# Optimization experiments

Measured on AMD Instinct MI355X. Metric: run time of the kernel, lower is better.

The kernel has to match this reference:

```python
import jax, jax.numpy as jnp
import numpy as np

B, S, HID = 2, 2048, 4096
NH, NKV = 32, 8
HD = HID // NH          # 128
GROUPS = NH // NKV      # 4


def rotate_half(x):
    x1, x2 = x[..., : x.shape[-1] // 2], x[..., x.shape[-1] // 2 :]
    return jnp.concatenate((-x2, x1), axis=-1)


def apply_rope(x, cos, sin):
    # x: (B,H,S,D); cos/sin: (B,S,D) -> (B,1,S,D)
    c = cos[:, None, :, :]
    s = sin[:, None, :, :]
    return x * c + rotate_half(x) * s


def setup_inputs() -> dict:
    key = jax.random.key(0)
    ks = jax.random.split(key, 12)
    scale = 1.0 / np.sqrt(HID)
    return {
        "hidden_states": jax.random.normal(ks[0], (B, S, HID), jnp.float32),
        "cos": jax.random.uniform(ks[1], (B, S, HD), jnp.float32),
        "sin": jax.random.uniform(ks[2], (B, S, HD), jnp.float32),
        "Wq": jax.random.normal(ks[3], (HID, NH * HD), jnp.float32) * scale,
        "bq": jax.random.normal(ks[4], (NH * HD,), jnp.float32) * 0.01,
        "Wk": jax.random.normal(ks[5], (HID, NKV * HD), jnp.float32) * scale,
        "bk": jax.random.normal(ks[6], (NKV * HD,), jnp.float32) * 0.01,
        "Wv": jax.random.normal(ks[7], (HID, NKV * HD), jnp.float32) * scale,
        "bv": jax.random.normal(ks[8], (NKV * HD,), jnp.float32) * 0.01,
        "Wo": jax.random.normal(ks[9], (NH * HD, HID), jnp.float32) * scale,
    }


def reference(hidden_states, cos, sin, Wq, bq, Wk, bk, Wv, bv, Wo):
    b, s, _ = hidden_states.shape
    q = (hidden_states @ Wq + bq).reshape(b, s, NH, HD).transpose(0, 2, 1, 3)
    k = (hidden_states @ Wk + bk).reshape(b, s, NKV, HD).transpose(0, 2, 1, 3)
    v = (hidden_states @ Wv + bv).reshape(b, s, NKV, HD).transpose(0, 2, 1, 3)
    q = apply_rope(q, cos, sin)
    k = apply_rope(k, cos, sin)
    # GQA: repeat_interleave along head dim
    k = jnp.repeat(k, GROUPS, axis=1)
    v = jnp.repeat(v, GROUPS, axis=1)
    scores = jnp.einsum("bhqd,bhkd->bhqk", q, k) / np.sqrt(HD).astype(np.float32)
    weights = jax.nn.softmax(scores, axis=-1)  # NOTE: no causal mask, per source
    out = jnp.einsum("bhqk,bhkd->bhqd", weights, v)
    out = out.transpose(0, 2, 1, 3).reshape(b, s, NH * HD)
    return out @ Wo
```

## Files before the change

kernel.cpp:

```cpp
#include <hip/hip_runtime.h>
#include <stdint.h>

#define Bz   2
#define Ss   2048
#define HID  4096
#define NH   32
#define NKV  8
#define HD   128
#define Mrows (Bz*Ss)
#define NQKV 6144

typedef __attribute__((ext_vector_type(8))) short b16x8;
typedef __attribute__((ext_vector_type(8))) _Float16 f16x8;
typedef __attribute__((ext_vector_type(4))) float f32x4;

__device__ __forceinline__ unsigned short f2bf(float f) {
  union { float f; uint32_t u; } v; v.f = f;
  uint32_t r = v.u + 0x7FFFu + ((v.u >> 16) & 1u);
  return (unsigned short)(r >> 16);
}

__device__ __forceinline__ void cp16(const void* g, void* l) {
  __builtin_amdgcn_global_load_lds(
      (const __attribute__((address_space(1))) void*)g,
      (__attribute__((address_space(3))) void*)l, 16, 0, 0);
}

__global__ __launch_bounds__(256) void cast_x(const float* __restrict__ x,
                                              unsigned short* __restrict__ o) {
  int i = blockIdx.x*256 + threadIdx.x;
  float4 v = ((const float4*)x)[i];
  ushort4 r; r.x = f2bf(v.x); r.y = f2bf(v.y); r.z = f2bf(v.z); r.w = f2bf(v.w);
  ((ushort4*)o)[i] = r;
}

__global__ __launch_bounds__(256) void wtrans(const float* __restrict__ W,
                                              unsigned short* __restrict__ Wt,
                                              int K, int N) {
  __shared__ float t[32][33];
  int n0 = blockIdx.x*32, k0 = blockIdx.y*32;
  int tx = threadIdx.x & 31, ty = threadIdx.x >> 5;
#pragma unroll
  for (int i = 0; i < 4; i++)
    t[ty + i*8][tx] = W[(size_t)(k0 + ty + i*8)*N + n0 + tx];
  __syncthreads();
#pragma unroll
  for (int i = 0; i < 4; i++)
    Wt[(size_t)(n0 + ty + i*8)*K + k0 + tx] = f2bf(t[tx][ty + i*8]);
}

__global__ __launch_bounds__(256) void bias_cat(const float* __restrict__ bq,
                                                const float* __restrict__ bk,
                                                const float* __restrict__ bv,
                                                float* __restrict__ o) {
  int i = blockIdx.x*256 + threadIdx.x;
  float v = (i < 4096) ? bq[i] : (i < 5120) ? bk[i-4096] : bv[i-5120];
  o[i] = v;
}

__global__ __launch_bounds__(256) void gemm_bt(const unsigned short* __restrict__ A,
                                               const unsigned short* __restrict__ Bt,
                                               const float* __restrict__ bias,
                                               float* __restrict__ C,
                                               int N, int K) {
  __shared__ short Al[128*32];
  __shared__ short Bl[128*32];
  const int tid = threadIdx.x;
  const int m0 = blockIdx.y * 128, n0 = blockIdx.x * 128;
  const int w = tid >> 6, lane = tid & 63;
  const int wy = w >> 1, wx = w & 1;
  const int lrow = lane & 15, quad = lane >> 4;
  const int wb = tid & 192;
  const int swz = (lrow >> 1) & 3;
  f32x4 acc[4][4] = {};
  for (int kk = 0; kk < K; kk += 32) {
    __syncthreads();
#pragma unroll
    for (int i = 0; i < 2; i++) {
      int c = i*256 + tid;
      int r = c >> 2, gc = (c & 3) ^ ((r >> 1) & 3);
      int cb = i*256 + wb;
      cp16(A  + (size_t)(m0 + r)*K + kk + gc*8, Al + cb*8);
      cp16(Bt + (size_t)(n0 + r)*K + kk + gc*8, Bl + cb*8);
    }
    __syncthreads();
    b16x8 af[4], bfr[4];
#pragma unroll
    for (int m = 0; m < 4; m++)
      af[m] = *(const b16x8*)(Al + (wy*64 + m*16 + lrow)*32 + (quad ^ swz)*8);
#pragma unroll
    for (int n = 0; n < 4; n++)
      bfr[n] = *(const b16x8*)(Bl + (wx*64 + n*16 + lrow)*32 + (quad ^ swz)*8);
#pragma unroll
    for (int m = 0; m < 4; m++)
#pragma unroll
      for (int n = 0; n < 4; n++)
        acc[m][n] = __builtin_amdgcn_mfma_f32_16x16x32_bf16(af[m], bfr[n], acc[m][n], 0, 0, 0);
  }
#pragma unroll
  for (int m = 0; m < 4; m++)
#pragma unroll
    for (int n = 0; n < 4; n++) {
      int col = n0 + wx*64 + n*16 + lrow;
      float bv = bias ? bias[col] : 0.0f;
#pragma unroll
      for (int r = 0; r < 4; r++) {
        int row = m0 + wy*64 + m*16 + quad*4 + r;
        C[(size_t)row*N + col] = acc[m][n][r] + bv;
      }
    }
}

__global__ __launch_bounds__(256) void rope(const float* __restrict__ X, int xstride, int colbase,
                                            const float* __restrict__ cp,
                                            const float* __restrict__ sp,
                                            unsigned short* __restrict__ o, int nh, float scale) {
  int tid = blockIdx.x*256 + threadIdx.x;
  int d = tid & 63;
  int h = (tid >> 6) % nh;
  int m = tid / (64*nh);
  int b = m >> 11, s = m & 2047;
  size_t xoff = (size_t)m*xstride + colbase + (size_t)h*HD + d;
  float x1 = X[xoff], x2 = X[xoff + 64];
  const float* cb = cp + ((size_t)b*Ss + s)*HD;
  const float* sb = sp + ((size_t)b*Ss + s)*HD;
  float o1 = (x1*cb[d]      - x2*sb[d])      * scale;
  float o2 = (x2*cb[d + 64] + x1*sb[d + 64]) * scale;
  unsigned short* ob = o + ((size_t)(b*nh + h)*Ss + s)*HD;
  ob[d]      = f2bf(o1);
  ob[d + 64] = f2bf(o2);
}

__global__ __launch_bounds__(256) void vprep(const float* __restrict__ Vf, int xstride, int colbase,
                                             _Float16* __restrict__ Vt) {
  __shared__ float t[32][33];
  int dt = blockIdx.x, st = blockIdx.y, bk = blockIdx.z;
  int b = bk >> 3, kvh = bk & 7;
  int tx = threadIdx.x & 31, ty = threadIdx.x >> 5;
#pragma unroll
  for (int i = 0; i < 4; i++) {
    int s = st*32 + ty + i*8;
    t[ty + i*8][tx] = Vf[(size_t)(b*Ss + s)*xstride + colbase + kvh*HD + dt*32 + tx];
  }
  __syncthreads();
#pragma unroll
  for (int i = 0; i < 4; i++) {
    int d = dt*32 + ty + i*8;
    Vt[((size_t)bk*HD + d)*Ss + st*32 + tx] = (_Float16)t[tx][ty + i*8];
  }
}

__global__ __launch_bounds__(256) void flash(const unsigned short* __restrict__ Qr,
                                             const unsigned short* __restrict__ Kr,
                                             const _Float16* __restrict__ Vt,
                                             unsigned short* __restrict__ AO) {
  __shared__ short Kl[64*128];
  __shared__ short Vl[144*64];
  __shared__ _Float16 Pl[4][16*72];
  const int qt = blockIdx.x, h = blockIdx.y, b = blockIdx.z;
  const int tid = threadIdx.x, w = tid >> 6, lane = tid & 63;
  const int lrow = lane & 15, quad = lane >> 4;
  const int wb = tid & 192;
  const int swz = lrow & 7;
  const int kvh = h >> 2;
  const unsigned short* Qb = Qr + ((size_t)(b*NH + h)*Ss + qt*64 + w*16)*HD;
  const unsigned short* Kb = Kr + ((size_t)(b*NKV + kvh)*Ss)*HD;
  const _Float16*       Vb = Vt + ((size_t)(b*NKV + kvh)*HD)*Ss;
  {
    int idx = tid*4;
    int row = 128 + (idx >> 6);
    unsigned short v = (row == 128) ? 0x3C00u : 0u;
    ushort4 vv; vv.x = v; vv.y = v; vv.z = v; vv.w = v;
    *(ushort4*)((unsigned short*)Vl + 128*64 + idx) = vv;
  }
  b16x8 qf[4];
#pragma unroll
  for (int t = 0; t < 4; t++)
    qf[t] = *(const b16x8*)(Qb + (size_t)lrow*HD + t*32 + quad*8);
  f32x4 o[8] = {};
  f32x4 ol = {};
  for (int kt = 0; kt < 32; kt++) {
    __syncthreads();
#pragma unroll
    for (int i = 0; i < 4; i++) {
      int c = i*256 + tid;
      int r = c >> 4, gc = (c & 15) ^ (r & 7);
      cp16(Kb + (size_t)(kt*64 + r)*HD + gc*8, Kl + (i*256 + wb)*8);
    }
#pragma unroll
    for (int i = 0; i < 4; i++) {
      int c = i*256 + tid;
      int r = c >> 3, gc = (c & 7) ^ (r & 7);
      cp16(Vb + (size_t)r*Ss + kt*64 + gc*8, Vl + (i*256 + wb)*8);
    }
    __syncthreads();
    f32x4 sc[4] = {};
#pragma unroll
    for (int t = 0; t < 4; t++)
#pragma unroll
      for (int n = 0; n < 4; n++) {
        b16x8 kf = *(const b16x8*)(Kl + (n*16 + lrow)*128 + ((t*4 + quad) ^ swz)*8);
        sc[n] = __builtin_amdgcn_mfma_f32_16x16x32_bf16(qf[t], kf, sc[n], 0, 0, 0);
      }
#pragma unroll
    for (int n = 0; n < 4; n++)
#pragma unroll
      for (int r = 0; r < 4; r++)
        Pl[w][(quad*4 + r)*72 + n*16 + lrow] = (_Float16)__builtin_amdgcn_exp2f(sc[n][r]);
#pragma unroll
    for (int st = 0; st < 2; st++) {
      f16x8 pf = *(const f16x8*)(&Pl[w][lrow*72 + st*32 + quad*8]);
#pragma unroll
      for (int n = 0; n < 8; n++) {
        f16x8 vf = *(const f16x8*)((const _Float16*)Vl + (n*16 + lrow)*64 + ((st*4 + quad) ^ swz)*8);
        o[n] = __builtin_amdgcn_mfma_f32_16x16x32_f16(pf, vf, o[n], 0, 0, 0);
      }
      f16x8 vf1 = *(const f16x8*)((const _Float16*)Vl + (128 + lrow)*64 + ((st*4 + quad) ^ swz)*8);
      ol = __builtin_amdgcn_mfma_f32_16x16x32_f16(pf, vf1, ol, 0, 0, 0);
    }
  }
  float rl[4];
#pragma unroll
  for (int r = 0; r < 4; r++)
    rl[r] = 1.0f / __shfl(ol[r], lane & 48);
  const int s0 = qt*64 + w*16;
#pragma unroll
  for (int n = 0; n < 8; n++)
#pragma unroll
    for (int r = 0; r < 4; r++) {
      int srow = s0 + quad*4 + r;
      float v = o[n][r] * rl[r];
      AO[((size_t)(b*Ss + srow))*HID + h*HD + n*16 + lrow] = f2bf(v);
    }
}

extern "C" void kernel_launch(void* const* d_in, const int* in_sizes, int n_in,
                              void* d_out, int out_size, void* d_ws, size_t ws_size,
                              hipStream_t stream) {
  (void)in_sizes; (void)n_in; (void)out_size; (void)ws_size;
  const float* hs   = (const float*)d_in[0];
  const float* cosp = (const float*)d_in[1];
  const float* sinp = (const float*)d_in[2];
  const float* Wq   = (const float*)d_in[3];
  const float* bq   = (const float*)d_in[4];
  const float* Wk   = (const float*)d_in[5];
  const float* bk   = (const float*)d_in[6];
  const float* Wv   = (const float*)d_in[7];
  const float* bv   = (const float*)d_in[8];
  const float* Wo   = (const float*)d_in[9];
  float* out = (float*)d_out;
  const float QSC = 0.12751742826919558f;

  char* p = (char*)d_ws;
  unsigned short* Xb   = (unsigned short*)p; p += (size_t)Mrows*HID*2;
  unsigned short* Wcat = (unsigned short*)p; p += (size_t)NQKV*HID*2;
  unsigned short* Wot  = (unsigned short*)p; p += (size_t)HID*HID*2;
  float* bcat = (float*)p; p += (size_t)NQKV*4;
  float* QKVf = (float*)p; p += (size_t)Mrows*NQKV*4;
  unsigned short* Qr = Xb;
  unsigned short* Kr = Wcat;
  _Float16*       Vt = (_Float16*)(Wcat + (size_t)(Bz*NKV)*Ss*HD);
  unsigned short* AO = (unsigned short*)QKVf;

  cast_x<<<Mrows*HID/1024, 256, 0, stream>>>(hs, Xb);
  wtrans<<<dim3(HID/32, HID/32),      256, 0, stream>>>(Wq, Wcat,                        HID, HID);
  wtrans<<<dim3((NKV*HD)/32, HID/32), 256, 0, stream>>>(Wk, Wcat + (size_t)4096*HID,     HID, NKV*HD);
  wtrans<<<dim3((NKV*HD)/32, HID/32), 256, 0, stream>>>(Wv, Wcat + (size_t)5120*HID,     HID, NKV*HD);
  wtrans<<<dim3(HID/32, HID/32),      256, 0, stream>>>(Wo, Wot, HID, HID);
  bias_cat<<<NQKV/256, 256, 0, stream>>>(bq, bk, bv, bcat);

  gemm_bt<<<dim3(NQKV/128, Mrows/128), 256, 0, stream>>>(Xb, Wcat, bcat, QKVf, NQKV, HID);

  rope<<<(Mrows*NH*64)/256,  256, 0, stream>>>(QKVf, NQKV, 0,    cosp, sinp, Qr, NH,  QSC);
  rope<<<(Mrows*NKV*64)/256, 256, 0, stream>>>(QKVf, NQKV, 4096, cosp, sinp, Kr, NKV, 1.0f);
  vprep<<<dim3(HD/32, Ss/32, Bz*NKV), 256, 0, stream>>>(QKVf, NQKV, 5120, Vt);

  flash<<<dim3(Ss/64, NH, Bz), 256, 0, stream>>>(Qr, Kr, Vt, AO);

  gemm_bt<<<dim3(HID/128, Mrows/128), 256, 0, stream>>>(AO, Wot, nullptr, out, HID, HID);
}
```

Baseline: 975.0 us.

## Rewrite GEMM with 256x256 tiles, double-buffered LDS, and XCD-aware block remap

The bf16 GEMM is restructured to use 512-thread blocks computing 256x256 output tiles with K-step 64. LDS is double-buffered so global-to-LDS async copies for tile t+2 overlap the MFMA work on the current tile, with explicit waitcnt and barriers. Block IDs are remapped across the eight XCDs to improve L2 locality, and setprio raises priority around the MFMA bursts. The larger tile increases register pressure (a 32-accumulator array per wave) and LDS use (128KB per block), which could limit occupancy. With K=4096, the QKV GEMM launches 24x16 blocks and the output GEMM 16x16 blocks, so wave quantization on the 256-CU device is a risk.

```diff
diff --git a/kernel.cpp b/kernel.cpp
--- a/kernel.cpp
+++ b/kernel.cpp
@@ -58,55 +58,102 @@
   o[i] = v;
 }
 
-__global__ __launch_bounds__(256) void gemm_bt(const unsigned short* __restrict__ A,
-                                               const unsigned short* __restrict__ Bt,
-                                               const float* __restrict__ bias,
-                                               float* __restrict__ C,
-                                               int N, int K) {
-  __shared__ short Al[128*32];
-  __shared__ short Bl[128*32];
+__global__ __launch_bounds__(512, 2) void gemm_bt(const unsigned short* __restrict__ A,
+                                                  const unsigned short* __restrict__ Bt,
+                                                  const float* __restrict__ bias,
+                                                  float* __restrict__ C,
+                                                  int N, int K) {
+  __shared__ short Al[2][256*64];
+  __shared__ short Bl[2][256*64];
   const int tid = threadIdx.x;
-  const int m0 = blockIdx.y * 128, n0 = blockIdx.x * 128;
   const int w = tid >> 6, lane = tid & 63;
-  const int wy = w >> 1, wx = w & 1;
+  const int wm = w >> 2, wn = w & 3;
   const int lrow = lane & 15, quad = lane >> 4;
-  const int wb = tid & 192;
-  const int swz = (lrow >> 1) & 3;
-  f32x4 acc[4][4] = {};
-  for (int kk = 0; kk < K; kk += 32) {
-    __syncthreads();
-#pragma unroll
-    for (int i = 0; i < 2; i++) {
-      int c = i*256 + tid;
-      int r = c >> 2, gc = (c & 3) ^ ((r >> 1) & 3);
-      int cb = i*256 + wb;
-      cp16(A  + (size_t)(m0 + r)*K + kk + gc*8, Al + cb*8);
-      cp16(Bt + (size_t)(n0 + r)*K + kk + gc*8, Bl + cb*8);
-    }
-    __syncthreads();
-    b16x8 af[4], bfr[4];
-#pragma unroll
-    for (int m = 0; m < 4; m++)
-      af[m] = *(const b16x8*)(Al + (wy*64 + m*16 + lrow)*32 + (quad ^ swz)*8);
-#pragma unroll
-    for (int n = 0; n < 4; n++)
-      bfr[n] = *(const b16x8*)(Bl + (wx*64 + n*16 + lrow)*32 + (quad ^ swz)*8);
-#pragma unroll
-    for (int m = 0; m < 4; m++)
-#pragma unroll
-      for (int n = 0; n < 4; n++)
-        acc[m][n] = __builtin_amdgcn_mfma_f32_16x16x32_bf16(af[m], bfr[n], acc[m][n], 0, 0, 0);
-  }
-#pragma unroll
-  for (int m = 0; m < 4; m++)
-#pragma unroll
-    for (int n = 0; n < 4; n++) {
-      int col = n0 + wx*64 + n*16 + lrow;
+  const int swz = lrow & 7;
+  int bid = blockIdx.y * gridDim.x + blockIdx.x;
+  const int nwg = gridDim.x * gridDim.y;
+  bid = (bid & 7) * (nwg >> 3) + (bid >> 3);
+  const int m0 = (bid / gridDim.x) * 256;
+  const int n0 = (bid % gridDim.x) * 256;
+  const int rr = tid >> 3;
+  const int gc = (tid & 7) ^ (rr & 7);
+  const unsigned short* ga = A  + (size_t)(m0 + rr)*K + gc*8;
+  const unsigned short* gb = Bt + (size_t)(n0 + rr)*K + gc*8;
+  short* la = &Al[0][0] + (size_t)w*512;
+  short* lb = &Bl[0][0] + (size_t)w*512;
+  const short* arow = &Al[0][0] + (wm*128 + lrow)*64;
+  const short* brow = &Bl[0][0] + (wn*64  + lrow)*64;
+  const int kc = (quad ^ swz) * 8;
+  const int NT = K >> 6;
+  f32x4 acc[8][4] = {};
+
+#define STAGE_T(buf, kt)                                                        \
+  {                                                                             \
+    _Pragma("unroll")                                                           \
+    for (int j = 0; j < 4; j++) {                                               \
+      cp16(ga + (size_t)(j*64)*K + (size_t)(kt)*64, la + (buf)*16384 + j*4096); \
+      cp16(gb + (size_t)(j*64)*K + (size_t)(kt)*64, lb + (buf)*16384 + j*4096); \
+    }                                                                           \
+  }
+
+  STAGE_T(0, 0);
+  STAGE_T(1, 1);
+  asm volatile("s_waitcnt vmcnt(8)" ::: "memory");
+  __builtin_amdgcn_s_barrier();
+  __builtin_amdgcn_sched_barrier(0);
+
+  for (int t = 0; t < NT; ++t) {
+    const int cb = (t & 1) * 16384;
+    b16x8 af[8], bfr[4];
+#pragma unroll
+    for (int mi = 0; mi < 8; mi++)
+      af[mi] = *(const b16x8*)(arow + cb + mi*1024 + kc);
+#pragma unroll
+    for (int ni = 0; ni < 4; ni++)
+      bfr[ni] = *(const b16x8*)(brow + cb + ni*1024 + kc);
+    __builtin_amdgcn_s_setprio(1);
+#pragma unroll
+    for (int mi = 0; mi < 8; mi++)
+#pragma unroll
+      for (int ni = 0; ni < 4; ni++)
+        acc[mi][ni] = __builtin_amdgcn_mfma_f32_16x16x32_bf16(af[mi], bfr[ni], acc[mi][ni], 0, 0, 0);
+    __builtin_amdgcn_s_setprio(0);
+    b16x8 af1[8], bf1[4];
+#pragma unroll
+    for (int mi = 0; mi < 8; mi++)
+      af1[mi] = *(const b16x8*)(arow + cb + mi*1024 + (kc ^ 32));
+#pragma unroll
+    for (int ni = 0; ni < 4; ni++)
+      bf1[ni] = *(const b16x8*)(brow + cb + ni*1024 + (kc ^ 32));
+    asm volatile("s_waitcnt lgkmcnt(0)" ::: "memory");
+    __builtin_amdgcn_s_barrier();
+    __builtin_amdgcn_sched_barrier(0);
+    if (t + 2 < NT) STAGE_T(t & 1, t + 2);
+    __builtin_amdgcn_sched_barrier(0);
+    __builtin_amdgcn_s_setprio(1);
+#pragma unroll
+    for (int mi = 0; mi < 8; mi++)
+#pragma unroll
+      for (int ni = 0; ni < 4; ni++)
+        acc[mi][ni] = __builtin_amdgcn_mfma_f32_16x16x32_bf16(af1[mi], bf1[ni], acc[mi][ni], 0, 0, 0);
+    __builtin_amdgcn_s_setprio(0);
+    if (t + 2 < NT) { asm volatile("s_waitcnt vmcnt(8)" ::: "memory"); }
+    else            { asm volatile("s_waitcnt vmcnt(0)" ::: "memory"); }
+    __builtin_amdgcn_s_barrier();
+    __builtin_amdgcn_sched_barrier(0);
+  }
+#undef STAGE_T
+
+#pragma unroll
+  for (int mi = 0; mi < 8; mi++)
+#pragma unroll
+    for (int ni = 0; ni < 4; ni++) {
+      int col = n0 + wn*64 + ni*16 + lrow;
       float bv = bias ? bias[col] : 0.0f;
 #pragma unroll
       for (int r = 0; r < 4; r++) {
-        int row = m0 + wy*64 + m*16 + quad*4 + r;
-        C[(size_t)row*N + col] = acc[m][n][r] + bv;
+        int row = m0 + wm*128 + mi*16 + quad*4 + r;
+        C[(size_t)row*N + col] = acc[mi][ni][r] + bv;
       }
     }
 }
@@ -269,7 +316,7 @@
   wtrans<<<dim3(HID/32, HID/32),      256, 0, stream>>>(Wo, Wot, HID, HID);
   bias_cat<<<NQKV/256, 256, 0, stream>>>(bq, bk, bv, bcat);
 
-  gemm_bt<<<dim3(NQKV/128, Mrows/128), 256, 0, stream>>>(Xb, Wcat, bcat, QKVf, NQKV, HID);
+  gemm_bt<<<dim3(NQKV/256, Mrows/256), 512, 0, stream>>>(Xb, Wcat, bcat, QKVf, NQKV, HID);
 
   rope<<<(Mrows*NH*64)/256,  256, 0, stream>>>(QKVf, NQKV, 0,    cosp, sinp, Qr, NH,  QSC);
   rope<<<(Mrows*NKV*64)/256, 256, 0, stream>>>(QKVf, NQKV, 4096, cosp, sinp, Kr, NKV, 1.0f);
@@ -277,5 +324,5 @@
 
   flash<<<dim3(Ss/64, NH, Bz), 256, 0, stream>>>(Qr, Kr, Vt, AO);
 
-  gemm_bt<<<dim3(HID/128, Mrows/128), 256, 0, stream>>>(AO, Wot, nullptr, out, HID, HID);
-}
+  gemm_bt<<<dim3(HID/256, Mrows/256), 512, 0, stream>>>(AO, Wot, nullptr, out, HID, HID);
+}
```

After: 864.1 us. 11.4% less time.
